# Optimization experiments

Measured on AMD Instinct MI355X. Metric: run time of the kernel, lower is better.

## Reference

```python
import jax, jax.numpy as jnp
import numpy as np

NEG = -1e30

def setup_inputs() -> dict:
    key = jax.random.key(0)
    k = jax.random.split(key, 6)
    B, Lc, Lq, D = 16, 2048, 256, 256
    c = jax.random.normal(k[0], (B, Lc, D), dtype=jnp.float32)
    q = jax.random.normal(k[1], (B, Lq, D), dtype=jnp.float32)
    c_mask = jnp.ones((B, Lc), dtype=jnp.float32)
    q_mask = jnp.ones((B, Lq), dtype=jnp.float32)
    # xavier-uniform-ish scale for the similarity weights
    lim = float(np.sqrt(6.0 / (D + 1)))
    cq_weight = jax.random.uniform(k[2], (1, 1, D), jnp.float32, -lim, lim)
    c_weight = jax.random.uniform(k[3], (1, D), jnp.float32, -lim, lim)
    q_weight = jax.random.uniform(k[4], (1, D), jnp.float32, -lim, lim)
    bias = jnp.zeros((1,), dtype=jnp.float32)
    return {"c": c, "q": q, "c_mask": c_mask, "q_mask": q_mask,
            "cq_weight": cq_weight, "c_weight": c_weight,
            "q_weight": q_weight, "bias": bias}

def _masked_softmax(logits, mask):
    # mask: 1=keep, 0=pad; broadcast over logits' leading dims
    x = logits * mask + (1.0 - mask) * NEG
    return jax.nn.softmax(x, axis=-1)

def reference(c, q, c_mask, q_mask, cq_weight, c_weight, q_weight, bias):
    # trilinear similarity S[b,i,j] = w_c.c_i + w_q.q_j + (c_i*w_cq).q_j + b
    s0 = jnp.einsum('bid,od->bio', c, c_weight)              # [B,Lc,1]
    s1 = jnp.einsum('bjd,od->boj', q, q_weight)              # [B,1,Lq]
    s2 = jnp.einsum('bid,bjd->bij', c * cq_weight, q)        # [B,Lc,Lq]
    S = s0 + s1 + s2 + bias                                  # [B,Lc,Lq]
    S1 = _masked_softmax(S, q_mask[:, None, :])              # softmax over q
    C2Q = jnp.einsum('bij,bjd->bid', S1, q)                  # [B,Lc,D]
    S2t = _masked_softmax(jnp.swapaxes(S, 1, 2), c_mask[:, None, :])  # [B,Lq,Lc]
    S2 = jnp.einsum('bij,bjk->bik', S1, S2t)                 # [B,Lc,Lc]
    Q2C = jnp.einsum('bik,bkd->bid', S2, c)                  # [B,Lc,D]
    return jnp.concatenate((c, C2Q, c * C2Q, c * Q2C), axis=-1)
```

## Files before the change

kernel.cpp:

```cpp
#include <hip/hip_runtime.h>
#include <hip/hip_bf16.h>

#define NB 16
#define LC 2048
#define LQ 256
#define DD 256
#define NEGINF -1e30f

typedef __attribute__((ext_vector_type(8))) short bf16x8;
typedef __attribute__((ext_vector_type(4))) float f32x4;

#define MFMA16(a, b, c) __builtin_amdgcn_mfma_f32_16x16x32_bf16((a), (b), (c), 0, 0, 0)

typedef const unsigned int __attribute__((address_space(1))) glb_u32;
typedef unsigned int __attribute__((address_space(3))) lds_u32;

__device__ __forceinline__ void gload_lds16(const void* g, void* l) {
    __builtin_amdgcn_global_load_lds((glb_u32*)g, (lds_u32*)l, 16, 0, 0);
}

__device__ __forceinline__ short f2b(float x) {
    unsigned u = __float_as_uint(x);
    unsigned r = (u + 0x7fffu + ((u >> 16) & 1u)) >> 16;
    return (short)r;
}
__device__ __forceinline__ float b2f(short s) {
    return __uint_as_float(((unsigned)(unsigned short)s) << 16);
}

__global__ __launch_bounds__(256) void prep_c(
        const float* __restrict__ c, const float* __restrict__ c_w,
        short* __restrict__ c16, float* __restrict__ s0c) {
    int row = blockIdx.x * 8 + (threadIdx.x >> 5);
    int k = threadIdx.x & 31;
    const float* src = c + (size_t)row * DD + k * 8;
    float4 v0 = *(const float4*)(src);
    float4 v1 = *(const float4*)(src + 4);
    float4 w0 = *(const float4*)(c_w + k * 8);
    float4 w1 = *(const float4*)(c_w + k * 8 + 4);
    float s = v0.x * w0.x + v0.y * w0.y + v0.z * w0.z + v0.w * w0.w
            + v1.x * w1.x + v1.y * w1.y + v1.z * w1.z + v1.w * w1.w;
    #pragma unroll
    for (int o = 16; o > 0; o >>= 1) s += __shfl_xor(s, o, 64);
    if (k == 0) s0c[row] = s;
    ushort4 o0, o1;
    o0.x = (unsigned short)f2b(v0.x); o0.y = (unsigned short)f2b(v0.y);
    o0.z = (unsigned short)f2b(v0.z); o0.w = (unsigned short)f2b(v0.w);
    o1.x = (unsigned short)f2b(v1.x); o1.y = (unsigned short)f2b(v1.y);
    o1.z = (unsigned short)f2b(v1.z); o1.w = (unsigned short)f2b(v1.w);
    ushort4* dst = (ushort4*)(c16 + (size_t)row * DD + k * 8);
    dst[0] = o0;
    dst[1] = o1;
}

__global__ __launch_bounds__(256) void prep_q(
        const float* __restrict__ q, const float* __restrict__ cqw,
        const float* __restrict__ q_w, const float* __restrict__ bias,
        short* __restrict__ qw16, short* __restrict__ qT16,
        float* __restrict__ s1q) {
    __shared__ float T[64][65];
    int b = blockIdx.y, j0 = blockIdx.x * 64, t = threadIdx.x;
    int dd = t & 63, rg = t >> 6;
    float acc[16];
    #pragma unroll
    for (int i = 0; i < 16; ++i) acc[i] = 0.f;
    for (int dc = 0; dc < 4; ++dc) {
        float wv = cqw[dc * 64 + dd];
        float qwv = q_w[dc * 64 + dd];
        #pragma unroll
        for (int rr = 0; rr < 16; ++rr) {
            int r = rg + 4 * rr;
            float v = q[((size_t)b * LQ + j0 + r) * DD + dc * 64 + dd];
            qw16[((size_t)b * LQ + j0 + r) * DD + dc * 64 + dd] = f2b(v * wv);
            acc[rr] += v * qwv;
            T[dd][r] = v;
        }
        __syncthreads();
        int jj = t & 63;
        for (int dw = t >> 6; dw < 64; dw += 4)
            qT16[((size_t)b * DD + dc * 64 + dw) * LQ + j0 + jj] = f2b(T[dw][jj]);
        __syncthreads();
    }
    float bv = bias[0];
    #pragma unroll
    for (int rr = 0; rr < 16; ++rr) {
        float s = acc[rr];
        #pragma unroll
        for (int o = 32; o > 0; o >>= 1) s += __shfl_xor(s, o, 64);
        if (dd == 0) s1q[b * LQ + j0 + rg + 4 * rr] = s + bv;
    }
}

__global__ __launch_bounds__(512) void k1_S(
        const short* __restrict__ c16, const short* __restrict__ qw16,
        const float* __restrict__ cmask, const float* __restrict__ qmask,
        const float* __restrict__ s0c, const float* __restrict__ s1q,
        short* __restrict__ Sb, float* __restrict__ pm, float* __restrict__ ps,
        float* __restrict__ rowC) {
    __shared__ short As[128 * 64];
    __shared__ short Bs[256 * 64];
    __shared__ float rmLds[128 * 4];
    __shared__ float rsLds[128 * 4];
    int b  = blockIdx.y;
    int i0 = blockIdx.x * 128;
    int t = threadIdx.x;
    int l = t & 63, w = t >> 6;
    int wr = w >> 2, wc = w & 3;

    f32x4 acc[4][4];
    #pragma unroll
    for (int m = 0; m < 4; ++m)
        #pragma unroll
        for (int n = 0; n < 4; ++n) acc[m][n] = (f32x4){0.f, 0.f, 0.f, 0.f};

    const short* Ag = c16  + ((size_t)b * LC + i0) * DD;
    const short* Bg = qw16 + ((size_t)b * LQ) * DD;
    int lrow = l >> 3;
    int lcolsw = ((l & 7) ^ lrow) * 8;

    for (int kt = 0; kt < DD; kt += 64) {
        __syncthreads();
        #pragma unroll
        for (int r = 0; r < 2; ++r) {
            int chunk = r * 8 + w;
            int row = chunk * 8 + lrow;
            gload_lds16(Ag + (size_t)row * DD + kt + lcolsw, As + chunk * 512);
        }
        #pragma unroll
        for (int r = 0; r < 4; ++r) {
            int chunk = r * 8 + w;
            int row = chunk * 8 + lrow;
            gload_lds16(Bg + (size_t)row * DD + kt + lcolsw, Bs + chunk * 512);
        }
        __syncthreads();
        #pragma unroll
        for (int kf = 0; kf < 2; ++kf) {
            bf16x8 a[4], bb[4];
            #pragma unroll
            for (int m = 0; m < 4; ++m) {
                int row = wr * 64 + m * 16 + (l & 15);
                int byte = row * 128 + kf * 64 + (l >> 4) * 16;
                a[m] = *(const bf16x8*)((const char*)As + (byte ^ ((row & 7) << 4)));
            }
            #pragma unroll
            for (int n = 0; n < 4; ++n) {
                int row = wc * 64 + n * 16 + (l & 15);
                int byte = row * 128 + kf * 64 + (l >> 4) * 16;
                bb[n] = *(const bf16x8*)((const char*)Bs + (byte ^ ((row & 7) << 4)));
            }
            #pragma unroll
            for (int m = 0; m < 4; ++m)
                #pragma unroll
                for (int n = 0; n < 4; ++n)
                    acc[m][n] = MFMA16(a[m], bb[n], acc[m][n]);
        }
    }

    float s1v[4], qmv[4], negq[4];
    #pragma unroll
    for (int n = 0; n < 4; ++n) {
        int j = wc * 64 + n * 16 + (l & 15);
        s1v[n] = s1q[b * LQ + j];
        qmv[n] = qmask[b * LQ + j];
        negq[n] = (1.f - qmv[n]) * NEGINF;
    }
    float s0r[4][4], cmr[4][4];
    #pragma unroll
    for (int m = 0; m < 4; ++m)
        #pragma unroll
        for (int reg = 0; reg < 4; ++reg) {
            int il = wr * 64 + m * 16 + (l >> 4) * 4 + reg;
            s0r[m][reg] = s0c[b * LC + i0 + il];
            cmr[m][reg] = cmask[b * LC + i0 + il];
        }
    #pragma unroll
    for (int m = 0; m < 4; ++m)
        #pragma unroll
        for (int n = 0; n < 4; ++n)
            #pragma unroll
            for (int reg = 0; reg < 4; ++reg) {
                float v = acc[m][n][reg] + s0r[m][reg] + s1v[n];
                short sb = f2b(v);
                int il = wr * 64 + m * 16 + (l >> 4) * 4 + reg;
                int j = wc * 64 + n * 16 + (l & 15);
                Sb[((size_t)b * LC + i0 + il) * LQ + j] = sb;
                acc[m][n][reg] = b2f(sb);
            }

    #pragma unroll
    for (int n = 0; n < 4; ++n) {
        float x2v[16];
        float mx = NEGINF;
        #pragma unroll
        for (int m = 0; m < 4; ++m)
            #pragma unroll
            for (int reg = 0; reg < 4; ++reg) {
                float cm = cmr[m][reg];
                float x2 = acc[m][n][reg] * cm + (1.f - cm) * NEGINF;
                x2v[m * 4 + reg] = x2;
                mx = fmaxf(mx, x2);
            }
        float ss = 0.f;
        #pragma unroll
        for (int e = 0; e < 16; ++e) ss += __expf(x2v[e] - mx);
        #pragma unroll
        for (int off = 16; off <= 32; off <<= 1) {
            float om = __shfl_xor(mx, off, 64);
            float os = __shfl_xor(ss, off, 64);
            float nm = fmaxf(mx, om);
            ss = ss * __expf(mx - nm) + os * __expf(om - nm);
            mx = nm;
        }
        if (l < 16) {
            int j = wc * 64 + n * 16 + l;
            size_t idx = ((size_t)b * 32 + blockIdx.x * 2 + wr) * LQ + j;
            pm[idx] = mx;
            ps[idx] = ss;
        }
    }

    #pragma unroll
    for (int m = 0; m < 4; ++m)
        #pragma unroll
        for (int reg = 0; reg < 4; ++reg) {
            float mx = NEGINF;
            #pragma unroll
            for (int n = 0; n < 4; ++n)
                mx = fmaxf(mx, fmaf(acc[m][n][reg], qmv[n], negq[n]));
            #pragma unroll
            for (int o = 1; o <= 8; o <<= 1) mx = fmaxf(mx, __shfl_xor(mx, o, 64));
            float ss = 0.f;
            #pragma unroll
            for (int n = 0; n < 4; ++n)
                ss += __expf(fmaf(acc[m][n][reg], qmv[n], negq[n]) - mx);
            #pragma unroll
            for (int o = 1; o <= 8; o <<= 1) ss += __shfl_xor(ss, o, 64);
            if ((l & 15) == 0) {
                int row = wr * 64 + m * 16 + (l >> 4) * 4 + reg;
                rmLds[row * 4 + wc] = mx;
                rsLds[row * 4 + wc] = ss;
            }
        }
    __syncthreads();
    if (t < 128) {
        float m0 = rmLds[t * 4 + 0], m1 = rmLds[t * 4 + 1];
        float m2 = rmLds[t * 4 + 2], m3 = rmLds[t * 4 + 3];
        float mm = fmaxf(fmaxf(m0, m1), fmaxf(m2, m3));
        float ss = rsLds[t * 4 + 0] * __expf(m0 - mm)
                 + rsLds[t * 4 + 1] * __expf(m1 - mm)
                 + rsLds[t * 4 + 2] * __expf(m2 - mm)
                 + rsLds[t * 4 + 3] * __expf(m3 - mm);
        rowC[b * LC + i0 + t] = mm + logf(ss);
    }
}

#define K3S 72
__global__ __launch_bounds__(256) void k3_A2C(
        const short* __restrict__ c16, const short* __restrict__ Sb,
        const float* __restrict__ cmask,
        const float* __restrict__ pm, const float* __restrict__ ps,
        float* __restrict__ p3) {
    __shared__ short As[128 * K3S];
    __shared__ short Bs[128 * K3S];
    __shared__ float colCs[128];
    int b  = blockIdx.z;
    int ks = blockIdx.y;
    int d0 = (blockIdx.x >> 1) * 128;
    int j0 = (blockIdx.x & 1) * 128;
    int t = threadIdx.x, l = t & 63, w = t >> 6;
    int wr = w >> 1, wc = w & 1;

    if (t < 128) {
        float m = NEGINF, s = 0.f;
        for (int ch = 0; ch < 32; ++ch) {
            float pmv = pm[((size_t)b * 32 + ch) * LQ + j0 + t];
            float psv = ps[((size_t)b * 32 + ch) * LQ + t + j0];
            float mn = fmaxf(m, pmv);
            s = s * __expf(m - mn) + psv * __expf(pmv - mn);
            m = mn;
        }
        colCs[t] = m + logf(s);
    }
    __syncthreads();

    f32x4 acc[4][4];
    #pragma unroll
    for (int m = 0; m < 4; ++m)
        #pragma unroll
        for (int n = 0; n < 4; ++n) acc[m][n] = (f32x4){0.f, 0.f, 0.f, 0.f};

    int ii = t >> 2;
    int c4 = (t & 3) * 8;

    for (int k0 = ks * 512; k0 < ks * 512 + 512; k0 += 64) {
        __syncthreads();
        float cm = cmask[b * LC + k0 + ii];
        float negc = (1.f - cm) * NEGINF;
        #pragma unroll
        for (int e = 0; e < 4; ++e) {
            int dpos = c4 + e * 32;
            bf16x8 av = *(const bf16x8*)(c16 +
                    ((size_t)(b * LC + k0 + ii)) * DD + d0 + dpos);
            #pragma unroll
            for (int g = 0; g < 8; ++g) As[(dpos + g) * K3S + ii] = av[g];

            int jpos = c4 + e * 32;
            bf16x8 sv8 = *(const bf16x8*)(Sb +
                    ((size_t)(b * LC + k0 + ii)) * LQ + j0 + jpos);
            #pragma unroll
            for (int g = 0; g < 8; ++g) {
                float p = __expf(fmaf(b2f(sv8[g]), cm, negc) - colCs[jpos + g]);
                Bs[(jpos + g) * K3S + ii] = f2b(p);
            }
        }
        __syncthreads();
        #pragma unroll
        for (int kf = 0; kf < 2; ++kf) {
            bf16x8 a[4], bb[4];
            #pragma unroll
            for (int m = 0; m < 4; ++m) {
                int row = wr * 64 + m * 16 + (l & 15);
                a[m] = *(const bf16x8*)((const char*)As +
                        row * (K3S * 2) + kf * 64 + (l >> 4) * 16);
            }
            #pragma unroll
            for (int n = 0; n < 4; ++n) {
                int row = wc * 64 + n * 16 + (l & 15);
                bb[n] = *(const bf16x8*)((const char*)Bs +
                        row * (K3S * 2) + kf * 64 + (l >> 4) * 16);
            }
            #pragma unroll
            for (int m = 0; m < 4; ++m)
                #pragma unroll
                for (int n = 0; n < 4; ++n)
                    acc[m][n] = MFMA16(a[m], bb[n], acc[m][n]);
        }
    }
    float* P = p3 + (((size_t)b * 4 + ks) * 4 + blockIdx.x) * 16384;
    #pragma unroll
    for (int m = 0; m < 4; ++m)
        #pragma unroll
        for (int n = 0; n < 4; ++n)
            #pragma unroll
            for (int reg = 0; reg < 4; ++reg) {
                int ld = wr * 64 + m * 16 + (l >> 4) * 4 + reg;
                int lj = wc * 64 + n * 16 + (l & 15);
                P[ld * 128 + lj] = acc[m][n][reg];
            }
}

__global__ __launch_bounds__(256) void k3r_reduce(
        const float* __restrict__ p3, short* __restrict__ A2CT) {
    int b = blockIdx.y;
    int linear = blockIdx.x * 256 + threadIdx.x;
    int d = linear >> 6;
    int j4 = (linear & 63) * 4;
    int tile = (d >> 7) * 2 + (j4 >> 7);
    int ld = d & 127, lj = j4 & 127;
    const float* base = p3 + (((size_t)b * 4) * 4 + tile) * 16384 + ld * 128 + lj;
    float4 s = {0.f, 0.f, 0.f, 0.f};
    #pragma unroll
    for (int ks = 0; ks < 4; ++ks) {
        float4 v = *(const float4*)(base + (size_t)ks * 4 * 16384);
        s.x += v.x; s.y += v.y; s.z += v.z; s.w += v.w;
    }
    short4 o;
    o.x = f2b(s.x); o.y = f2b(s.y); o.z = f2b(s.z); o.w = f2b(s.w);
    *(short4*)(A2CT + ((size_t)b * DD + d) * LQ + j4) = o;
}

__global__ __launch_bounds__(256) void k4_out(
        const short* __restrict__ Sb, const short* __restrict__ qT16,
        const short* __restrict__ A2CT, const float* __restrict__ c,
        const float* __restrict__ qmask, const float* __restrict__ rowC,
        float* __restrict__ out) {
    int b = blockIdx.y, i0 = blockIdx.x * 64;
    int t = threadIdx.x, l = t & 63, w = t >> 6;
    int d0w = w * 64;

    float rC[4];
    #pragma unroll
    for (int m = 0; m < 4; ++m)
        rC[m] = rowC[b * LC + i0 + m * 16 + (l & 15)];

    f32x4 acc1[4][4], acc2[4][4];
    #pragma unroll
    for (int m = 0; m < 4; ++m)
        #pragma unroll
        for (int n = 0; n < 4; ++n) {
            acc1[m][n] = (f32x4){0.f, 0.f, 0.f, 0.f};
            acc2[m][n] = (f32x4){0.f, 0.f, 0.f, 0.f};
        }
    const short* Sr  = Sb   + ((size_t)b * LC + i0) * LQ;
    const short* qTb = qT16 + (size_t)b * DD * LQ;
    const short* aTb = A2CT + (size_t)b * DD * LQ;

    for (int kf = 0; kf < 8; ++kf) {
        int j8 = kf * 32 + (l >> 4) * 8;
        float4 qa = *(const float4*)(qmask + b * LQ + j8);
        float4 qb2 = *(const float4*)(qmask + b * LQ + j8 + 4);
        float qm8[8] = {qa.x, qa.y, qa.z, qa.w, qb2.x, qb2.y, qb2.z, qb2.w};
        bf16x8 a[4];
        #pragma unroll
        for (int m = 0; m < 4; ++m) {
            bf16x8 s8 = *(const bf16x8*)(Sr + (size_t)(m * 16 + (l & 15)) * LQ + j8);
            #pragma unroll
            for (int g = 0; g < 8; ++g) {
                float x = fmaf(b2f(s8[g]), qm8[g], (1.f - qm8[g]) * NEGINF) - rC[m];
                a[m][g] = f2b(__expf(x));
            }
        }
        #pragma unroll
        for (int n = 0; n < 4; ++n) {
            int d = d0w + n * 16 + (l & 15);
            size_t off = (size_t)d * LQ + j8;
            bf16x8 bq = *(const bf16x8*)(qTb + off);
            bf16x8 ba = *(const bf16x8*)(aTb + off);
            #pragma unroll
            for (int m = 0; m < 4; ++m) {
                acc1[m][n] = MFMA16(a[m], bq, acc1[m][n]);
                acc2[m][n] = MFMA16(a[m], ba, acc2[m][n]);
            }
        }
    }
    #pragma unroll
    for (int m = 0; m < 4; ++m)
        #pragma unroll
        for (int n = 0; n < 4; ++n)
            #pragma unroll
            for (int reg = 0; reg < 4; ++reg) {
                int i = i0 + m * 16 + (l >> 4) * 4 + reg;
                int d = d0w + n * 16 + (l & 15);
                float cv = c[((size_t)b * LC + i) * DD + d];
                size_t ob = ((size_t)b * LC + i) * (size_t)(4 * DD);
                float v1 = acc1[m][n][reg], v2 = acc2[m][n][reg];
                out[ob + d]           = cv;
                out[ob + 256 + d]     = v1;
                out[ob + 512 + d]     = cv * v1;
                out[ob + 768 + d]     = cv * v2;
            }
}

extern "C" void kernel_launch(void* const* d_in, const int* in_sizes, int n_in,
                              void* d_out, int out_size, void* d_ws, size_t ws_size,
                              hipStream_t stream) {
    const float* c     = (const float*)d_in[0];
    const float* q     = (const float*)d_in[1];
    const float* cmask = (const float*)d_in[2];
    const float* qmask = (const float*)d_in[3];
    const float* cqw   = (const float*)d_in[4];
    const float* c_w   = (const float*)d_in[5];
    const float* q_w   = (const float*)d_in[6];
    const float* bias  = (const float*)d_in[7];
    float* out = (float*)d_out;

    char* w = (char*)d_ws;
    short* Sb    = (short*)(w);
    short* c16   = (short*)(w + 16777216);
    short* qw16  = (short*)(w + 33554432);
    short* qT16  = (short*)(w + 35651584);
    short* A2CT  = (short*)(w + 37748736);
    float* s0c   = (float*)(w + 39845888);
    float* s1q   = (float*)(w + 39976960);
    float* pm    = (float*)(w + 39993344);
    float* ps    = (float*)(w + 40517632);
    float* p3    = (float*)(w + 41041920);
    float* rowC  = (float*)(w + 57819136);

    prep_c<<<dim3(NB * LC / 8), dim3(256), 0, stream>>>(c, c_w, c16, s0c);
    prep_q<<<dim3(LQ / 64, NB), dim3(256), 0, stream>>>(
        q, cqw, q_w, bias, qw16, qT16, s1q);
    k1_S<<<dim3(LC / 128, NB), dim3(512), 0, stream>>>(
        c16, qw16, cmask, qmask, s0c, s1q, Sb, pm, ps, rowC);
    k3_A2C<<<dim3(4, 4, NB), dim3(256), 0, stream>>>(
        c16, Sb, cmask, pm, ps, p3);
    k3r_reduce<<<dim3(64, NB), dim3(256), 0, stream>>>(p3, A2CT);
    k4_out<<<dim3(LC / 64, NB), dim3(256), 0, stream>>>(
        Sb, qT16, A2CT, c, qmask, rowC, out);
}
```

Before: 121.0 us.

## Precompute softmax probabilities and transposed layouts, drop split-K A2C reduction

Result: slower. 146.6 us (+21.2%).

```diff
diff --git a/kernel.cpp b/kernel.cpp
--- a/kernel.cpp
+++ b/kernel.cpp
@@ -30,27 +30,38 @@
 
 __global__ __launch_bounds__(256) void prep_c(
         const float* __restrict__ c, const float* __restrict__ c_w,
-        short* __restrict__ c16, float* __restrict__ s0c) {
-    int row = blockIdx.x * 8 + (threadIdx.x >> 5);
-    int k = threadIdx.x & 31;
-    const float* src = c + (size_t)row * DD + k * 8;
-    float4 v0 = *(const float4*)(src);
-    float4 v1 = *(const float4*)(src + 4);
-    float4 w0 = *(const float4*)(c_w + k * 8);
-    float4 w1 = *(const float4*)(c_w + k * 8 + 4);
-    float s = v0.x * w0.x + v0.y * w0.y + v0.z * w0.z + v0.w * w0.w
-            + v1.x * w1.x + v1.y * w1.y + v1.z * w1.z + v1.w * w1.w;
-    #pragma unroll
-    for (int o = 16; o > 0; o >>= 1) s += __shfl_xor(s, o, 64);
-    if (k == 0) s0c[row] = s;
-    ushort4 o0, o1;
-    o0.x = (unsigned short)f2b(v0.x); o0.y = (unsigned short)f2b(v0.y);
-    o0.z = (unsigned short)f2b(v0.z); o0.w = (unsigned short)f2b(v0.w);
-    o1.x = (unsigned short)f2b(v1.x); o1.y = (unsigned short)f2b(v1.y);
-    o1.z = (unsigned short)f2b(v1.z); o1.w = (unsigned short)f2b(v1.w);
-    ushort4* dst = (ushort4*)(c16 + (size_t)row * DD + k * 8);
-    dst[0] = o0;
-    dst[1] = o1;
+        short* __restrict__ c16, short* __restrict__ cT16,
+        float* __restrict__ s0c) {
+    __shared__ float T[64][65];
+    int b = blockIdx.y, i0 = blockIdx.x * 64, t = threadIdx.x;
+    int dd = t & 63, rg = t >> 6;
+    float acc[16];
+    #pragma unroll
+    for (int i = 0; i < 16; ++i) acc[i] = 0.f;
+    for (int dc = 0; dc < 4; ++dc) {
+        float cwv = c_w[dc * 64 + dd];
+        #pragma unroll
+        for (int rr = 0; rr < 16; ++rr) {
+            int r = rg + 4 * rr;
+            float v = c[((size_t)b * LC + i0 + r) * DD + dc * 64 + dd];
+            c16[((size_t)b * LC + i0 + r) * DD + dc * 64 + dd] = f2b(v);
+            acc[rr] += v * cwv;
+            T[dd][r] = v;
+        }
+        __syncthreads();
+        int jj = t & 63;
+        for (int dw = t >> 6; dw < 64; dw += 4)
+            cT16[((size_t)b * DD + dc * 64 + dw) * (size_t)LC + i0 + jj] =
+                f2b(T[dw][jj]);
+        __syncthreads();
+    }
+    #pragma unroll
+    for (int rr = 0; rr < 16; ++rr) {
+        float s = acc[rr];
+        #pragma unroll
+        for (int o = 32; o > 0; o >>= 1) s += __shfl_xor(s, o, 64);
+        if (dd == 0) s0c[(size_t)b * LC + i0 + rg + 4 * rr] = s;
+    }
 }
 
 __global__ __launch_bounds__(256) void prep_q(
@@ -95,12 +106,13 @@
         const short* __restrict__ c16, const short* __restrict__ qw16,
         const float* __restrict__ cmask, const float* __restrict__ qmask,
         const float* __restrict__ s0c, const float* __restrict__ s1q,
-        short* __restrict__ Sb, float* __restrict__ pm, float* __restrict__ ps,
-        float* __restrict__ rowC) {
+        short* __restrict__ P1b, short* __restrict__ STb,
+        float* __restrict__ pm, float* __restrict__ ps) {
     __shared__ short As[128 * 64];
     __shared__ short Bs[256 * 64];
     __shared__ float rmLds[128 * 4];
     __shared__ float rsLds[128 * 4];
+    __shared__ float rowCLds[128];
     int b  = blockIdx.y;
     int i0 = blockIdx.x * 128;
     int t = threadIdx.x;
@@ -180,15 +192,12 @@
             #pragma unroll
             for (int reg = 0; reg < 4; ++reg) {
                 float v = acc[m][n][reg] + s0r[m][reg] + s1v[n];
-                short sb = f2b(v);
-                int il = wr * 64 + m * 16 + (l >> 4) * 4 + reg;
-                int j = wc * 64 + n * 16 + (l & 15);
-                Sb[((size_t)b * LC + i0 + il) * LQ + j] = sb;
-                acc[m][n][reg] = b2f(sb);
+                acc[m][n][reg] = b2f(f2b(v));
             }
 
     #pragma unroll
     for (int n = 0; n < 4; ++n) {
+        int j = wc * 64 + n * 16 + (l & 15);
         float x2v[16];
         float mx = NEGINF;
         #pragma unroll
@@ -200,6 +209,16 @@
                 x2v[m * 4 + reg] = x2;
                 mx = fmaxf(mx, x2);
             }
+        #pragma unroll
+        for (int m = 0; m < 4; ++m) {
+            short4 st;
+            st.x = f2b(x2v[m * 4 + 0]);
+            st.y = f2b(x2v[m * 4 + 1]);
+            st.z = f2b(x2v[m * 4 + 2]);
+            st.w = f2b(x2v[m * 4 + 3]);
+            *(short4*)(STb + ((size_t)b * LQ + j) * (size_t)LC +
+                       i0 + wr * 64 + m * 16 + (l >> 4) * 4) = st;
+        }
         float ss = 0.f;
         #pragma unroll
         for (int e = 0; e < 16; ++e) ss += __expf(x2v[e] - mx);
@@ -212,8 +231,7 @@
             mx = nm;
         }
         if (l < 16) {
-            int j = wc * 64 + n * 16 + l;
-            size_t idx = ((size_t)b * 32 + blockIdx.x * 2 + wr) * LQ + j;
+            size_t idx = ((size_t)b * 32 + blockIdx.x * 2 + wr) * LQ + wc * 64 + n * 16 + l;
             pm[idx] = mx;
             ps[idx] = ss;
         }
@@ -250,31 +268,40 @@
                  + rsLds[t * 4 + 1] * __expf(m1 - mm)
                  + rsLds[t * 4 + 2] * __expf(m2 - mm)
                  + rsLds[t * 4 + 3] * __expf(m3 - mm);
-        rowC[b * LC + i0 + t] = mm + logf(ss);
-    }
-}
-
-#define K3S 72
-__global__ __launch_bounds__(256) void k3_A2C(
-        const short* __restrict__ c16, const short* __restrict__ Sb,
-        const float* __restrict__ cmask,
-        const float* __restrict__ pm, const float* __restrict__ ps,
-        float* __restrict__ p3) {
-    __shared__ short As[128 * K3S];
-    __shared__ short Bs[128 * K3S];
-    __shared__ float colCs[128];
-    int b  = blockIdx.z;
-    int ks = blockIdx.y;
-    int d0 = (blockIdx.x >> 1) * 128;
-    int j0 = (blockIdx.x & 1) * 128;
-    int t = threadIdx.x, l = t & 63, w = t >> 6;
-    int wr = w >> 1, wc = w & 1;
-
-    if (t < 128) {
+        rowCLds[t] = mm + logf(ss);
+    }
+    __syncthreads();
+
+    float rC[4][4];
+    #pragma unroll
+    for (int m = 0; m < 4; ++m)
+        #pragma unroll
+        for (int reg = 0; reg < 4; ++reg)
+            rC[m][reg] = rowCLds[wr * 64 + m * 16 + (l >> 4) * 4 + reg];
+    #pragma unroll
+    for (int m = 0; m < 4; ++m)
+        #pragma unroll
+        for (int n = 0; n < 4; ++n)
+            #pragma unroll
+            for (int reg = 0; reg < 4; ++reg) {
+                float p = __expf(fmaf(acc[m][n][reg], qmv[n], negq[n]) - rC[m][reg]);
+                int il = wr * 64 + m * 16 + (l >> 4) * 4 + reg;
+                int j = wc * 64 + n * 16 + (l & 15);
+                P1b[((size_t)b * LC + i0 + il) * LQ + j] = f2b(p);
+            }
+}
+
+__global__ __launch_bounds__(256) void kP(
+        short* __restrict__ STb,
+        const float* __restrict__ pm, const float* __restrict__ ps) {
+    __shared__ float colCs[16];
+    int b = blockIdx.y, j0 = blockIdx.x * 16;
+    int t = threadIdx.x;
+    if (t < 16) {
         float m = NEGINF, s = 0.f;
         for (int ch = 0; ch < 32; ++ch) {
             float pmv = pm[((size_t)b * 32 + ch) * LQ + j0 + t];
-            float psv = ps[((size_t)b * 32 + ch) * LQ + t + j0];
+            float psv = ps[((size_t)b * 32 + ch) * LQ + j0 + t];
             float mn = fmaxf(m, pmv);
             s = s * __expf(m - mn) + psv * __expf(pmv - mn);
             m = mn;
@@ -282,107 +309,76 @@
         colCs[t] = m + logf(s);
     }
     __syncthreads();
-
-    f32x4 acc[4][4];
-    #pragma unroll
-    for (int m = 0; m < 4; ++m)
-        #pragma unroll
-        for (int n = 0; n < 4; ++n) acc[m][n] = (f32x4){0.f, 0.f, 0.f, 0.f};
-
-    int ii = t >> 2;
-    int c4 = (t & 3) * 8;
-
-    for (int k0 = ks * 512; k0 < ks * 512 + 512; k0 += 64) {
-        __syncthreads();
-        float cm = cmask[b * LC + k0 + ii];
-        float negc = (1.f - cm) * NEGINF;
-        #pragma unroll
-        for (int e = 0; e < 4; ++e) {
-            int dpos = c4 + e * 32;
-            bf16x8 av = *(const bf16x8*)(c16 +
-                    ((size_t)(b * LC + k0 + ii)) * DD + d0 + dpos);
-            #pragma unroll
-            for (int g = 0; g < 8; ++g) As[(dpos + g) * K3S + ii] = av[g];
-
-            int jpos = c4 + e * 32;
-            bf16x8 sv8 = *(const bf16x8*)(Sb +
-                    ((size_t)(b * LC + k0 + ii)) * LQ + j0 + jpos);
-            #pragma unroll
-            for (int g = 0; g < 8; ++g) {
-                float p = __expf(fmaf(b2f(sv8[g]), cm, negc) - colCs[jpos + g]);
-                Bs[(jpos + g) * K3S + ii] = f2b(p);
-            }
-        }
-        __syncthreads();
-        #pragma unroll
-        for (int kf = 0; kf < 2; ++kf) {
-            bf16x8 a[4], bb[4];
-            #pragma unroll
-            for (int m = 0; m < 4; ++m) {
-                int row = wr * 64 + m * 16 + (l & 15);
-                a[m] = *(const bf16x8*)((const char*)As +
-                        row * (K3S * 2) + kf * 64 + (l >> 4) * 16);
-            }
-            #pragma unroll
-            for (int n = 0; n < 4; ++n) {
-                int row = wc * 64 + n * 16 + (l & 15);
-                bb[n] = *(const bf16x8*)((const char*)Bs +
-                        row * (K3S * 2) + kf * 64 + (l >> 4) * 16);
-            }
-            #pragma unroll
-            for (int m = 0; m < 4; ++m)
-                #pragma unroll
-                for (int n = 0; n < 4; ++n)
-                    acc[m][n] = MFMA16(a[m], bb[n], acc[m][n]);
-        }
-    }
-    float* P = p3 + (((size_t)b * 4 + ks) * 4 + blockIdx.x) * 16384;
-    #pragma unroll
-    for (int m = 0; m < 4; ++m)
-        #pragma unroll
-        for (int n = 0; n < 4; ++n)
+    int r = t >> 4;
+    int ib = (t & 15) * 8;
+    float cC = colCs[r];
+    short* row = STb + ((size_t)b * LQ + j0 + r) * (size_t)LC;
+    #pragma unroll
+    for (int it = 0; it < 16; ++it) {
+        int i = ib + it * 128;
+        bf16x8 v = *(const bf16x8*)(row + i);
+        #pragma unroll
+        for (int g = 0; g < 8; ++g)
+            v[g] = f2b(__expf(b2f(v[g]) - cC));
+        *(bf16x8*)(row + i) = v;
+    }
+}
+
+__global__ __launch_bounds__(256) void k3_A2C(
+        const short* __restrict__ cT16, const short* __restrict__ P2T,
+        short* __restrict__ A2CT) {
+    int b = blockIdx.z;
+    int d0 = blockIdx.x * 64;
+    int j0 = blockIdx.y * 64;
+    int t = threadIdx.x, l = t & 63, w = t >> 6;
+    int wr = w >> 1, wc = w & 1;
+
+    f32x4 acc[2][2];
+    #pragma unroll
+    for (int m = 0; m < 2; ++m)
+        #pragma unroll
+        for (int n = 0; n < 2; ++n) acc[m][n] = (f32x4){0.f, 0.f, 0.f, 0.f};
+
+    const short* Ab = cT16 + ((size_t)b * DD + d0 + wr * 32 + (l & 15)) * (size_t)LC;
+    const short* Bb = P2T  + ((size_t)b * LQ + j0 + wc * 32 + (l & 15)) * (size_t)LC;
+    int ks0 = (l >> 4) * 8;
+
+    #pragma unroll 4
+    for (int kf = 0; kf < 64; ++kf) {
+        int ki = kf * 32 + ks0;
+        bf16x8 a[2], bb[2];
+        #pragma unroll
+        for (int m = 0; m < 2; ++m)
+            a[m] = *(const bf16x8*)(Ab + (size_t)(m * 16) * LC + ki);
+        #pragma unroll
+        for (int n = 0; n < 2; ++n)
+            bb[n] = *(const bf16x8*)(Bb + (size_t)(n * 16) * LC + ki);
+        #pragma unroll
+        for (int m = 0; m < 2; ++m)
+            #pragma unroll
+            for (int n = 0; n < 2; ++n)
+                acc[m][n] = MFMA16(a[m], bb[n], acc[m][n]);
+    }
+    #pragma unroll
+    for (int m = 0; m < 2; ++m)
+        #pragma unroll
+        for (int n = 0; n < 2; ++n)
             #pragma unroll
             for (int reg = 0; reg < 4; ++reg) {
-                int ld = wr * 64 + m * 16 + (l >> 4) * 4 + reg;
-                int lj = wc * 64 + n * 16 + (l & 15);
-                P[ld * 128 + lj] = acc[m][n][reg];
-            }
-}
-
-__global__ __launch_bounds__(256) void k3r_reduce(
-        const float* __restrict__ p3, short* __restrict__ A2CT) {
-    int b = blockIdx.y;
-    int linear = blockIdx.x * 256 + threadIdx.x;
-    int d = linear >> 6;
-    int j4 = (linear & 63) * 4;
-    int tile = (d >> 7) * 2 + (j4 >> 7);
-    int ld = d & 127, lj = j4 & 127;
-    const float* base = p3 + (((size_t)b * 4) * 4 + tile) * 16384 + ld * 128 + lj;
-    float4 s = {0.f, 0.f, 0.f, 0.f};
-    #pragma unroll
-    for (int ks = 0; ks < 4; ++ks) {
-        float4 v = *(const float4*)(base + (size_t)ks * 4 * 16384);
-        s.x += v.x; s.y += v.y; s.z += v.z; s.w += v.w;
-    }
-    short4 o;
-    o.x = f2b(s.x); o.y = f2b(s.y); o.z = f2b(s.z); o.w = f2b(s.w);
-    *(short4*)(A2CT + ((size_t)b * DD + d) * LQ + j4) = o;
+                int d = d0 + wr * 32 + m * 16 + (l >> 4) * 4 + reg;
+                int j = j0 + wc * 32 + n * 16 + (l & 15);
+                A2CT[((size_t)b * DD + d) * LQ + j] = f2b(acc[m][n][reg]);
+            }
 }
 
 __global__ __launch_bounds__(256) void k4_out(
-        const short* __restrict__ Sb, const short* __restrict__ qT16,
+        const short* __restrict__ P1b, const short* __restrict__ qT16,
         const short* __restrict__ A2CT, const float* __restrict__ c,
-        const float* __restrict__ qmask, const float* __restrict__ rowC,
         float* __restrict__ out) {
     int b = blockIdx.y, i0 = blockIdx.x * 64;
     int t = threadIdx.x, l = t & 63, w = t >> 6;
     int d0w = w * 64;
 
-    float rC[4];
-    #pragma unroll
-    for (int m = 0; m < 4; ++m)
-        rC[m] = rowC[b * LC + i0 + m * 16 + (l & 15)];
-
     f32x4 acc1[4][4], acc2[4][4];
     #pragma unroll
     for (int m = 0; m < 4; ++m)
@@ -391,25 +387,17 @@
             acc1[m][n] = (f32x4){0.f, 0.f, 0.f, 0.f};
             acc2[m][n] = (f32x4){0.f, 0.f, 0.f, 0.f};
         }
-    const short* Sr  = Sb   + ((size_t)b * LC + i0) * LQ;
+    const short* Sr  = P1b  + ((size_t)b * LC + i0) * LQ;
     const short* qTb = qT16 + (size_t)b * DD * LQ;
     const short* aTb = A2CT + (size_t)b * DD * LQ;
 
+    #pragma unroll 2
     for (int kf = 0; kf < 8; ++kf) {
         int j8 = kf * 32 + (l >> 4) * 8;
-        float4 qa = *(const float4*)(qmask + b * LQ + j8);
-        float4 qb2 = *(const float4*)(qmask + b * LQ + j8 + 4);
-        float qm8[8] = {qa.x, qa.y, qa.z, qa.w, qb2.x, qb2.y, qb2.z, qb2.w};
         bf16x8 a[4];
         #pragma unroll
-        for (int m = 0; m < 4; ++m) {
-            bf16x8 s8 = *(const bf16x8*)(Sr + (size_t)(m * 16 + (l & 15)) * LQ + j8);
-            #pragma unroll
-            for (int g = 0; g < 8; ++g) {
-                float x = fmaf(b2f(s8[g]), qm8[g], (1.f - qm8[g]) * NEGINF) - rC[m];
-                a[m][g] = f2b(__expf(x));
-            }
-        }
+        for (int m = 0; m < 4; ++m)
+            a[m] = *(const bf16x8*)(Sr + (size_t)(m * 16 + (l & 15)) * LQ + j8);
         #pragma unroll
         for (int n = 0; n < 4; ++n) {
             int d = d0w + n * 16 + (l & 15);
@@ -455,26 +443,25 @@
     float* out = (float*)d_out;
 
     char* w = (char*)d_ws;
-    short* Sb    = (short*)(w);
-    short* c16   = (short*)(w + 16777216);
-    short* qw16  = (short*)(w + 33554432);
-    short* qT16  = (short*)(w + 35651584);
-    short* A2CT  = (short*)(w + 37748736);
-    float* s0c   = (float*)(w + 39845888);
-    float* s1q   = (float*)(w + 39976960);
-    float* pm    = (float*)(w + 39993344);
-    float* ps    = (float*)(w + 40517632);
-    float* p3    = (float*)(w + 41041920);
-    float* rowC  = (float*)(w + 57819136);
-
-    prep_c<<<dim3(NB * LC / 8), dim3(256), 0, stream>>>(c, c_w, c16, s0c);
+    short* P1b   = (short*)(w);
+    short* STb   = (short*)(w + 16777216);
+    short* c16   = (short*)(w + 33554432);
+    short* cT16  = (short*)(w + 50331648);
+    short* qw16  = (short*)(w + 67108864);
+    short* qT16  = (short*)(w + 69206016);
+    short* A2CT  = (short*)(w + 71303168);
+    float* s0c   = (float*)(w + 73400320);
+    float* s1q   = (float*)(w + 73531392);
+    float* pm    = (float*)(w + 73547776);
+    float* ps    = (float*)(w + 74072064);
+
+    prep_c<<<dim3(LC / 64, NB), dim3(256), 0, stream>>>(c, c_w, c16, cT16, s0c);
     prep_q<<<dim3(LQ / 64, NB), dim3(256), 0, stream>>>(
         q, cqw, q_w, bias, qw16, qT16, s1q);
     k1_S<<<dim3(LC / 128, NB), dim3(512), 0, stream>>>(
-        c16, qw16, cmask, qmask, s0c, s1q, Sb, pm, ps, rowC);
-    k3_A2C<<<dim3(4, 4, NB), dim3(256), 0, stream>>>(
-        c16, Sb, cmask, pm, ps, p3);
-    k3r_reduce<<<dim3(64, NB), dim3(256), 0, stream>>>(p3, A2CT);
+        c16, qw16, cmask, qmask, s0c, s1q, P1b, STb, pm, ps);
+    kP<<<dim3(LQ / 16, NB), dim3(256), 0, stream>>>(STb, pm, ps);
+    k3_A2C<<<dim3(DD / 64, LQ / 64, NB), dim3(256), 0, stream>>>(cT16, STb, A2CT);
     k4_out<<<dim3(LC / 64, NB), dim3(256), 0, stream>>>(
-        Sb, qT16, A2CT, c, qmask, rowC, out);
-}
+        P1b, qT16, A2CT, c, out);
+}
```

## Store row-softmax probabilities instead of logits and factor column normalization

Applied to the files above, without the earlier changes.

New measurement: 118.8 us. Within noise of the previous version (-1.8%).

```diff
diff --git a/kernel.cpp b/kernel.cpp
--- a/kernel.cpp
+++ b/kernel.cpp
@@ -28,66 +28,69 @@
     return __uint_as_float(((unsigned)(unsigned short)s) << 16);
 }
 
-__global__ __launch_bounds__(256) void prep_c(
-        const float* __restrict__ c, const float* __restrict__ c_w,
-        short* __restrict__ c16, float* __restrict__ s0c) {
-    int row = blockIdx.x * 8 + (threadIdx.x >> 5);
-    int k = threadIdx.x & 31;
-    const float* src = c + (size_t)row * DD + k * 8;
-    float4 v0 = *(const float4*)(src);
-    float4 v1 = *(const float4*)(src + 4);
-    float4 w0 = *(const float4*)(c_w + k * 8);
-    float4 w1 = *(const float4*)(c_w + k * 8 + 4);
-    float s = v0.x * w0.x + v0.y * w0.y + v0.z * w0.z + v0.w * w0.w
-            + v1.x * w1.x + v1.y * w1.y + v1.z * w1.z + v1.w * w1.w;
-    #pragma unroll
-    for (int o = 16; o > 0; o >>= 1) s += __shfl_xor(s, o, 64);
-    if (k == 0) s0c[row] = s;
-    ushort4 o0, o1;
-    o0.x = (unsigned short)f2b(v0.x); o0.y = (unsigned short)f2b(v0.y);
-    o0.z = (unsigned short)f2b(v0.z); o0.w = (unsigned short)f2b(v0.w);
-    o1.x = (unsigned short)f2b(v1.x); o1.y = (unsigned short)f2b(v1.y);
-    o1.z = (unsigned short)f2b(v1.z); o1.w = (unsigned short)f2b(v1.w);
-    ushort4* dst = (ushort4*)(c16 + (size_t)row * DD + k * 8);
-    dst[0] = o0;
-    dst[1] = o1;
-}
-
-__global__ __launch_bounds__(256) void prep_q(
-        const float* __restrict__ q, const float* __restrict__ cqw,
+#define NCB (NB * LC / 8)
+__global__ __launch_bounds__(256) void prep(
+        const float* __restrict__ c, const float* __restrict__ q,
+        const float* __restrict__ c_w, const float* __restrict__ cqw,
         const float* __restrict__ q_w, const float* __restrict__ bias,
+        short* __restrict__ c16, float* __restrict__ s0c,
         short* __restrict__ qw16, short* __restrict__ qT16,
         float* __restrict__ s1q) {
     __shared__ float T[64][65];
-    int b = blockIdx.y, j0 = blockIdx.x * 64, t = threadIdx.x;
-    int dd = t & 63, rg = t >> 6;
-    float acc[16];
-    #pragma unroll
-    for (int i = 0; i < 16; ++i) acc[i] = 0.f;
-    for (int dc = 0; dc < 4; ++dc) {
-        float wv = cqw[dc * 64 + dd];
-        float qwv = q_w[dc * 64 + dd];
+    int t = threadIdx.x;
+    if (blockIdx.x < NCB) {
+        int row = blockIdx.x * 8 + (t >> 5);
+        int k = t & 31;
+        const float* src = c + (size_t)row * DD + k * 8;
+        float4 v0 = *(const float4*)(src);
+        float4 v1 = *(const float4*)(src + 4);
+        float4 w0 = *(const float4*)(c_w + k * 8);
+        float4 w1 = *(const float4*)(c_w + k * 8 + 4);
+        float s = v0.x * w0.x + v0.y * w0.y + v0.z * w0.z + v0.w * w0.w
+                + v1.x * w1.x + v1.y * w1.y + v1.z * w1.z + v1.w * w1.w;
+        #pragma unroll
+        for (int o = 16; o > 0; o >>= 1) s += __shfl_xor(s, o, 64);
+        if (k == 0) s0c[row] = s;
+        ushort4 o0, o1;
+        o0.x = (unsigned short)f2b(v0.x); o0.y = (unsigned short)f2b(v0.y);
+        o0.z = (unsigned short)f2b(v0.z); o0.w = (unsigned short)f2b(v0.w);
+        o1.x = (unsigned short)f2b(v1.x); o1.y = (unsigned short)f2b(v1.y);
+        o1.z = (unsigned short)f2b(v1.z); o1.w = (unsigned short)f2b(v1.w);
+        ushort4* dst = (ushort4*)(c16 + (size_t)row * DD + k * 8);
+        dst[0] = o0;
+        dst[1] = o1;
+    } else {
+        int idx = blockIdx.x - NCB;
+        int b = idx >> 2, j0 = (idx & 3) * 64;
+        int dd = t & 63, rg = t >> 6;
+        float acc[16];
+        #pragma unroll
+        for (int i = 0; i < 16; ++i) acc[i] = 0.f;
+        for (int dc = 0; dc < 4; ++dc) {
+            float wv = cqw[dc * 64 + dd];
+            float qwv = q_w[dc * 64 + dd];
+            #pragma unroll
+            for (int rr = 0; rr < 16; ++rr) {
+                int r = rg + 4 * rr;
+                float v = q[((size_t)b * LQ + j0 + r) * DD + dc * 64 + dd];
+                qw16[((size_t)b * LQ + j0 + r) * DD + dc * 64 + dd] = f2b(v * wv);
+                acc[rr] += v * qwv;
+                T[dd][r] = v;
+            }
+            __syncthreads();
+            int jj = t & 63;
+            for (int dw = t >> 6; dw < 64; dw += 4)
+                qT16[((size_t)b * DD + dc * 64 + dw) * LQ + j0 + jj] = f2b(T[dw][jj]);
+            __syncthreads();
+        }
+        float bv = bias[0];
         #pragma unroll
         for (int rr = 0; rr < 16; ++rr) {
-            int r = rg + 4 * rr;
-            float v = q[((size_t)b * LQ + j0 + r) * DD + dc * 64 + dd];
-            qw16[((size_t)b * LQ + j0 + r) * DD + dc * 64 + dd] = f2b(v * wv);
-            acc[rr] += v * qwv;
-            T[dd][r] = v;
-        }
-        __syncthreads();
-        int jj = t & 63;
-        for (int dw = t >> 6; dw < 64; dw += 4)
-            qT16[((size_t)b * DD + dc * 64 + dw) * LQ + j0 + jj] = f2b(T[dw][jj]);
-        __syncthreads();
-    }
-    float bv = bias[0];
-    #pragma unroll
-    for (int rr = 0; rr < 16; ++rr) {
-        float s = acc[rr];
-        #pragma unroll
-        for (int o = 32; o > 0; o >>= 1) s += __shfl_xor(s, o, 64);
-        if (dd == 0) s1q[b * LQ + j0 + rg + 4 * rr] = s + bv;
+            float s = acc[rr];
+            #pragma unroll
+            for (int o = 32; o > 0; o >>= 1) s += __shfl_xor(s, o, 64);
+            if (dd == 0) s1q[b * LQ + j0 + rg + 4 * rr] = s + bv;
+        }
     }
 }
 
@@ -95,12 +98,13 @@
         const short* __restrict__ c16, const short* __restrict__ qw16,
         const float* __restrict__ cmask, const float* __restrict__ qmask,
         const float* __restrict__ s0c, const float* __restrict__ s1q,
-        short* __restrict__ Sb, float* __restrict__ pm, float* __restrict__ ps,
-        float* __restrict__ rowC) {
+        short* __restrict__ P1b, float* __restrict__ rowC,
+        float* __restrict__ pm, float* __restrict__ ps) {
     __shared__ short As[128 * 64];
     __shared__ short Bs[256 * 64];
     __shared__ float rmLds[128 * 4];
     __shared__ float rsLds[128 * 4];
+    __shared__ float rowCLds[128];
     int b  = blockIdx.y;
     int i0 = blockIdx.x * 128;
     int t = threadIdx.x;
@@ -180,11 +184,7 @@
             #pragma unroll
             for (int reg = 0; reg < 4; ++reg) {
                 float v = acc[m][n][reg] + s0r[m][reg] + s1v[n];
-                short sb = f2b(v);
-                int il = wr * 64 + m * 16 + (l >> 4) * 4 + reg;
-                int j = wc * 64 + n * 16 + (l & 15);
-                Sb[((size_t)b * LC + i0 + il) * LQ + j] = sb;
-                acc[m][n][reg] = b2f(sb);
+                acc[m][n][reg] = b2f(f2b(v));
             }
 
     #pragma unroll
@@ -212,8 +212,7 @@
             mx = nm;
         }
         if (l < 16) {
-            int j = wc * 64 + n * 16 + l;
-            size_t idx = ((size_t)b * 32 + blockIdx.x * 2 + wr) * LQ + j;
+            size_t idx = ((size_t)b * 32 + blockIdx.x * 2 + wr) * LQ + wc * 64 + n * 16 + l;
             pm[idx] = mx;
             ps[idx] = ss;
         }
@@ -250,19 +249,38 @@
                  + rsLds[t * 4 + 1] * __expf(m1 - mm)
                  + rsLds[t * 4 + 2] * __expf(m2 - mm)
                  + rsLds[t * 4 + 3] * __expf(m3 - mm);
-        rowC[b * LC + i0 + t] = mm + logf(ss);
-    }
+        float rc = mm + logf(ss);
+        rowCLds[t] = rc;
+        rowC[(size_t)b * LC + i0 + t] = rc;
+    }
+    __syncthreads();
+
+    float rCv[4][4];
+    #pragma unroll
+    for (int m = 0; m < 4; ++m)
+        #pragma unroll
+        for (int reg = 0; reg < 4; ++reg)
+            rCv[m][reg] = rowCLds[wr * 64 + m * 16 + (l >> 4) * 4 + reg];
+    #pragma unroll
+    for (int m = 0; m < 4; ++m)
+        #pragma unroll
+        for (int n = 0; n < 4; ++n)
+            #pragma unroll
+            for (int reg = 0; reg < 4; ++reg) {
+                float p = __expf(fmaf(acc[m][n][reg], qmv[n], negq[n]) - rCv[m][reg]);
+                int il = wr * 64 + m * 16 + (l >> 4) * 4 + reg;
+                int j = wc * 64 + n * 16 + (l & 15);
+                P1b[((size_t)b * LC + i0 + il) * LQ + j] = f2b(p);
+            }
 }
 
 #define K3S 72
 __global__ __launch_bounds__(256) void k3_A2C(
-        const short* __restrict__ c16, const short* __restrict__ Sb,
-        const float* __restrict__ cmask,
-        const float* __restrict__ pm, const float* __restrict__ ps,
+        const short* __restrict__ c16, const short* __restrict__ P1b,
+        const float* __restrict__ cmask, const float* __restrict__ rowC,
         float* __restrict__ p3) {
     __shared__ short As[128 * K3S];
     __shared__ short Bs[128 * K3S];
-    __shared__ float colCs[128];
     int b  = blockIdx.z;
     int ks = blockIdx.y;
     int d0 = (blockIdx.x >> 1) * 128;
@@ -270,19 +288,6 @@
     int t = threadIdx.x, l = t & 63, w = t >> 6;
     int wr = w >> 1, wc = w & 1;
 
-    if (t < 128) {
-        float m = NEGINF, s = 0.f;
-        for (int ch = 0; ch < 32; ++ch) {
-            float pmv = pm[((size_t)b * 32 + ch) * LQ + j0 + t];
-            float psv = ps[((size_t)b * 32 + ch) * LQ + t + j0];
-            float mn = fmaxf(m, pmv);
-            s = s * __expf(m - mn) + psv * __expf(pmv - mn);
-            m = mn;
-        }
-        colCs[t] = m + logf(s);
-    }
-    __syncthreads();
-
     f32x4 acc[4][4];
     #pragma unroll
     for (int m = 0; m < 4; ++m)
@@ -294,8 +299,7 @@
 
     for (int k0 = ks * 512; k0 < ks * 512 + 512; k0 += 64) {
         __syncthreads();
-        float cm = cmask[b * LC + k0 + ii];
-        float negc = (1.f - cm) * NEGINF;
+        float wgt = cmask[b * LC + k0 + ii] * __expf(rowC[(size_t)b * LC + k0 + ii]);
         #pragma unroll
         for (int e = 0; e < 4; ++e) {
             int dpos = c4 + e * 32;
@@ -305,13 +309,11 @@
             for (int g = 0; g < 8; ++g) As[(dpos + g) * K3S + ii] = av[g];
 
             int jpos = c4 + e * 32;
-            bf16x8 sv8 = *(const bf16x8*)(Sb +
+            bf16x8 p8 = *(const bf16x8*)(P1b +
                     ((size_t)(b * LC + k0 + ii)) * LQ + j0 + jpos);
             #pragma unroll
-            for (int g = 0; g < 8; ++g) {
-                float p = __expf(fmaf(b2f(sv8[g]), cm, negc) - colCs[jpos + g]);
-                Bs[(jpos + g) * K3S + ii] = f2b(p);
-            }
+            for (int g = 0; g < 8; ++g)
+                Bs[(jpos + g) * K3S + ii] = f2b(b2f(p8[g]) * wgt);
         }
         __syncthreads();
         #pragma unroll
@@ -350,9 +352,25 @@
 }
 
 __global__ __launch_bounds__(256) void k3r_reduce(
-        const float* __restrict__ p3, short* __restrict__ A2CT) {
+        const float* __restrict__ p3,
+        const float* __restrict__ pm, const float* __restrict__ ps,
+        short* __restrict__ A2CT) {
+    __shared__ float colCs[256];
     int b = blockIdx.y;
-    int linear = blockIdx.x * 256 + threadIdx.x;
+    int t = threadIdx.x;
+    {
+        float m = NEGINF, s = 0.f;
+        for (int ch = 0; ch < 32; ++ch) {
+            float pmv = pm[((size_t)b * 32 + ch) * LQ + t];
+            float psv = ps[((size_t)b * 32 + ch) * LQ + t];
+            float mn = fmaxf(m, pmv);
+            s = s * __expf(m - mn) + psv * __expf(pmv - mn);
+            m = mn;
+        }
+        colCs[t] = m + logf(s);
+    }
+    __syncthreads();
+    int linear = blockIdx.x * 256 + t;
     int d = linear >> 6;
     int j4 = (linear & 63) * 4;
     int tile = (d >> 7) * 2 + (j4 >> 7);
@@ -364,25 +382,23 @@
         float4 v = *(const float4*)(base + (size_t)ks * 4 * 16384);
         s.x += v.x; s.y += v.y; s.z += v.z; s.w += v.w;
     }
+    s.x *= __expf(-colCs[j4 + 0]);
+    s.y *= __expf(-colCs[j4 + 1]);
+    s.z *= __expf(-colCs[j4 + 2]);
+    s.w *= __expf(-colCs[j4 + 3]);
     short4 o;
     o.x = f2b(s.x); o.y = f2b(s.y); o.z = f2b(s.z); o.w = f2b(s.w);
     *(short4*)(A2CT + ((size_t)b * DD + d) * LQ + j4) = o;
 }
 
 __global__ __launch_bounds__(256) void k4_out(
-        const short* __restrict__ Sb, const short* __restrict__ qT16,
+        const short* __restrict__ P1b, const short* __restrict__ qT16,
         const short* __restrict__ A2CT, const float* __restrict__ c,
-        const float* __restrict__ qmask, const float* __restrict__ rowC,
         float* __restrict__ out) {
     int b = blockIdx.y, i0 = blockIdx.x * 64;
     int t = threadIdx.x, l = t & 63, w = t >> 6;
     int d0w = w * 64;
 
-    float rC[4];
-    #pragma unroll
-    for (int m = 0; m < 4; ++m)
-        rC[m] = rowC[b * LC + i0 + m * 16 + (l & 15)];
-
     f32x4 acc1[4][4], acc2[4][4];
     #pragma unroll
     for (int m = 0; m < 4; ++m)
@@ -391,25 +407,17 @@
             acc1[m][n] = (f32x4){0.f, 0.f, 0.f, 0.f};
             acc2[m][n] = (f32x4){0.f, 0.f, 0.f, 0.f};
         }
-    const short* Sr  = Sb   + ((size_t)b * LC + i0) * LQ;
+    const short* Sr  = P1b  + ((size_t)b * LC + i0) * LQ;
     const short* qTb = qT16 + (size_t)b * DD * LQ;
     const short* aTb = A2CT + (size_t)b * DD * LQ;
 
+    #pragma unroll 2
     for (int kf = 0; kf < 8; ++kf) {
         int j8 = kf * 32 + (l >> 4) * 8;
-        float4 qa = *(const float4*)(qmask + b * LQ + j8);
-        float4 qb2 = *(const float4*)(qmask + b * LQ + j8 + 4);
-        float qm8[8] = {qa.x, qa.y, qa.z, qa.w, qb2.x, qb2.y, qb2.z, qb2.w};
         bf16x8 a[4];
         #pragma unroll
-        for (int m = 0; m < 4; ++m) {
-            bf16x8 s8 = *(const bf16x8*)(Sr + (size_t)(m * 16 + (l & 15)) * LQ + j8);
-            #pragma unroll
-            for (int g = 0; g < 8; ++g) {
-                float x = fmaf(b2f(s8[g]), qm8[g], (1.f - qm8[g]) * NEGINF) - rC[m];
-                a[m][g] = f2b(__expf(x));
-            }
-        }
+        for (int m = 0; m < 4; ++m)
+            a[m] = *(const bf16x8*)(Sr + (size_t)(m * 16 + (l & 15)) * LQ + j8);
         #pragma unroll
         for (int n = 0; n < 4; ++n) {
             int d = d0w + n * 16 + (l & 15);
@@ -455,7 +463,7 @@
     float* out = (float*)d_out;
 
     char* w = (char*)d_ws;
-    short* Sb    = (short*)(w);
+    short* P1b   = (short*)(w);
     short* c16   = (short*)(w + 16777216);
     short* qw16  = (short*)(w + 33554432);
     short* qT16  = (short*)(w + 35651584);
@@ -464,17 +472,16 @@
     float* s1q   = (float*)(w + 39976960);
     float* pm    = (float*)(w + 39993344);
     float* ps    = (float*)(w + 40517632);
-    float* p3    = (float*)(w + 41041920);
-    float* rowC  = (float*)(w + 57819136);
-
-    prep_c<<<dim3(NB * LC / 8), dim3(256), 0, stream>>>(c, c_w, c16, s0c);
-    prep_q<<<dim3(LQ / 64, NB), dim3(256), 0, stream>>>(
-        q, cqw, q_w, bias, qw16, qT16, s1q);
+    float* rowC  = (float*)(w + 41041920);
+    float* p3    = (float*)(w + 41172992);
+
+    prep<<<dim3(NCB + NB * LQ / 64), dim3(256), 0, stream>>>(
+        c, q, c_w, cqw, q_w, bias, c16, s0c, qw16, qT16, s1q);
     k1_S<<<dim3(LC / 128, NB), dim3(512), 0, stream>>>(
-        c16, qw16, cmask, qmask, s0c, s1q, Sb, pm, ps, rowC);
+        c16, qw16, cmask, qmask, s0c, s1q, P1b, rowC, pm, ps);
     k3_A2C<<<dim3(4, 4, NB), dim3(256), 0, stream>>>(
-        c16, Sb, cmask, pm, ps, p3);
-    k3r_reduce<<<dim3(64, NB), dim3(256), 0, stream>>>(p3, A2CT);
+        c16, P1b, cmask, rowC, p3);
+    k3r_reduce<<<dim3(64, NB), dim3(256), 0, stream>>>(p3, pm, ps, A2CT);
     k4_out<<<dim3(LC / 64, NB), dim3(256), 0, stream>>>(
-        Sb, qT16, A2CT, c, qmask, rowC, out);
-}
+        P1b, qT16, A2CT, c, out);
+}
```
